# Performance work log

Hardware: AMD Instinct MI355X
Metric: run time of the kernel (lower is better)

Reference implementation:

```python
import jax, jax.numpy as jnp
from jax import lax
import numpy as np

OUTS = [5, 1, 2, 2, 1, 1, 1, 1]  # heatmap, conf, dxy, wh, dist, offset, severity, surface
OFFS = np.concatenate([[0], np.cumsum(OUTS)])
BN_EPS = 1e-5


def setup_inputs() -> dict:
    key = jax.random.key(0)
    ks = jax.random.split(key, 10)
    N, C, Hf, Wf = 16, 576, 12, 20
    f = jax.random.normal(ks[0], (N, C, Hf, Wf), jnp.float32)
    det_w1 = jax.random.normal(ks[1], (8, C, C, 3, 3), jnp.float32) * 0.02
    det_bn_g = 1.0 + 0.1 * jax.random.normal(ks[2], (8, C), jnp.float32)
    det_bn_b = 0.1 * jax.random.normal(ks[3], (8, C), jnp.float32)
    det_bn_m = 0.1 * jax.random.normal(ks[4], (8, C), jnp.float32)
    det_bn_v = jax.random.uniform(ks[5], (8, C), jnp.float32) + 0.5
    det_w2 = jax.random.normal(ks[6], (14, C), jnp.float32) * 0.05
    det_b2 = jax.random.normal(ks[7], (14,), jnp.float32) * 0.05
    lin_W = jax.random.normal(ks[8], (10, C), jnp.float32) * 0.05
    lin_b = jnp.zeros((10,), jnp.float32)
    return dict(f=f, det_w1=det_w1, det_bn_g=det_bn_g, det_bn_b=det_bn_b,
                det_bn_m=det_bn_m, det_bn_v=det_bn_v, det_w2=det_w2, det_b2=det_b2,
                lin_W=lin_W, lin_b=lin_b, frame_w=640, frame_h=384)


def _head(f, w1, g, b, m, v, w2, b2):
    # conv3x3 (no bias) -> BN (inference) -> SiLU -> conv1x1
    dn = ('NCHW', 'OIHW', 'NCHW')
    h = lax.conv_general_dilated(f, w1, (1, 1), 'SAME', dimension_numbers=dn)
    scale = g * lax.rsqrt(v + BN_EPS)
    h = h * scale[None, :, None, None] + (b - m * scale)[None, :, None, None]
    h = h * jax.nn.sigmoid(h)  # SiLU
    return jnp.einsum('nchw,oc->nohw', h, w2) + b2[None, :, None, None]


def _forward(f, det_w1, det_bn_g, det_bn_b, det_bn_m, det_bn_v, det_w2, det_b2,
             lin_W, lin_b, frame_w, frame_h, max_dets=20):
    N, C, Hf, Wf = f.shape
    eps = 1e-5
    # ---- legacy single-hazard head from pooled features ----
    f1 = f.mean(axis=(2, 3))                      # [N, 576]  (AdaptiveAvgPool2d(1))
    lin = f1 @ lin_W.T + lin_b                    # [N, 10]
    conf = jnp.clip(jax.nn.sigmoid(lin[:, 0:1]), eps, 1.0 - eps)
    type_log = lin[:, 1:6]
    dist_m = jax.nn.sigmoid(lin[:, 6:7]) * 3.0
    offset = jnp.tanh(lin[:, 7:8])
    severity = jnp.clip(jax.nn.sigmoid(lin[:, 8:9]), eps, 1.0 - eps)
    surface = jnp.clip(jax.nn.sigmoid(lin[:, 9:10]), eps, 1.0 - eps)
    type_id = jnp.argmax(type_log, axis=1, keepdims=True).astype(f.dtype)
    single_out = jnp.concatenate([conf, type_id, dist_m, offset, severity, surface], axis=1)

    # ---- dense per-pixel heads ----
    maps = []
    for i in range(8):
        o0, o1 = int(OFFS[i]), int(OFFS[i + 1])
        maps.append(_head(f, det_w1[i], det_bn_g[i], det_bn_b[i],
                          det_bn_m[i], det_bn_v[i], det_w2[o0:o1], det_b2[o0:o1]))
    heat = jax.nn.sigmoid(maps[0])                # [N,5,H,W]
    conf_d = jax.nn.sigmoid(maps[1])              # [N,1,H,W]
    dxy = jax.nn.sigmoid(maps[2])                 # [N,2,H,W]
    wh = jax.nn.sigmoid(maps[3])                  # [N,2,H,W]
    dist = jax.nn.sigmoid(maps[4]) * 3.0          # [N,1,H,W]
    offsm = jnp.tanh(maps[5])
    sev = jax.nn.sigmoid(maps[6])
    surf = jax.nn.sigmoid(maps[7])

    # ---- per-class topk decode ----
    score_flat = (conf_d * heat).reshape(N, 5, Hf * Wf)
    k = min(max_dets, Hf * Wf)
    topk_scores, topk_idx = lax.top_k(score_flat, k)          # [N,5,k]
    top_scores = topk_scores.reshape(N, -1)                    # [N,5k]
    top_class = jnp.broadcast_to(jnp.arange(5, dtype=f.dtype)[None, :, None], (N, 5, k)).reshape(N, -1)
    idx_flat = topk_idx.reshape(N, -1)                          # [N,5k]
    y_idx = (idx_flat // Wf).astype(f.dtype)
    x_idx = (idx_flat % Wf).astype(f.dtype)

    g1 = lambda m: jnp.take_along_axis(m.reshape(N, -1), idx_flat, axis=1)
    gx, gy = g1(dxy[:, 0]), g1(dxy[:, 1])
    gw, gh = g1(wh[:, 0]), g1(wh[:, 1])
    gdist, goffs = g1(dist), g1(offsm)
    gsev, gsurf = g1(sev), g1(surf)

    stride_x = frame_w / Wf
    stride_y = frame_h / Hf
    cx = jnp.clip(x_idx + gx, 0, Wf - 1) * stride_x
    cy = jnp.clip(y_idx + gy, 0, Hf - 1) * stride_y
    bw = jnp.clip(gw, 0, 1) * frame_w
    bh = jnp.clip(gh, 0, 1) * frame_h
    x1 = jnp.clip(cx - bw / 2, 0, frame_w - 1)
    y1 = jnp.clip(cy - bh / 2, 0, frame_h - 1)
    x2 = jnp.clip(cx + bw / 2, 0, frame_w - 1)
    y2 = jnp.clip(cy + bh / 2, 0, frame_h - 1)

    dets = jnp.stack([top_scores, top_class, gdist, goffs, gsev, gsurf, x1, y1, x2, y2], axis=-1)  # [N,5k,10]
    order = jnp.argsort(dets[:, :, 2], axis=-1)   # ascending distance (nearest first)
    dets_sorted = jnp.take_along_axis(dets, order[:, :, None], axis=1)
    dets_out = dets_sorted[:, :max_dets, :]        # [N,K,10]
    return single_out, dets_out


def reference(f, det_w1, det_bn_g, det_bn_b, det_bn_m, det_bn_v, det_w2, det_b2,
              lin_W, lin_b, frame_w, frame_h):
    return _forward(f, det_w1, det_bn_g, det_bn_b, det_bn_m, det_bn_v,
                    det_w2, det_b2, lin_W, lin_b, frame_w, frame_h)
```

## Files before the change

kernel.cpp:

```cpp
#include <hip/hip_runtime.h>
#include <math.h>

#define NB 16
#define CC 576
#define HH 12
#define WW 20
#define PP 240
#define MM 3840
#define NHEAD 8
#define HALO 22

typedef __attribute__((ext_vector_type(8))) short short8;
typedef __attribute__((ext_vector_type(4))) float floatx4;
typedef unsigned short ushort_t;

__device__ __forceinline__ float sigmoidf_(float x) {
    return 1.0f / (1.0f + expf(-x));
}
__device__ __forceinline__ unsigned short f2bf(float x) {
    union { float f; unsigned u; } v; v.f = x;
    unsigned r = v.u + 0x7fff + ((v.u >> 16) & 1);
    return (unsigned short)(r >> 16);
}
__device__ __forceinline__ float bf2f(unsigned short b) {
    union { float f; unsigned u; } v; v.u = ((unsigned)b) << 16;
    return v.f;
}

__device__ __forceinline__ void gl_lds16(const ushort_t* g, ushort_t* l) {
    __builtin_amdgcn_global_load_lds(
        (const __attribute__((address_space(1))) void*)g,
        (__attribute__((address_space(3))) void*)l, 16, 0, 0);
}

#define FENCED_BARRIER() do {                   \
    asm volatile("" ::: "memory");              \
    __builtin_amdgcn_sched_barrier(0);          \
    __builtin_amdgcn_s_barrier();               \
    __builtin_amdgcn_sched_barrier(0);          \
    asm volatile("" ::: "memory");              \
} while (0)

__global__ __launch_bounds__(256) void k_single(const float* __restrict__ f1sum,
                                                const float* __restrict__ linW,
                                                const float* __restrict__ linb,
                                                float* __restrict__ out) {
    int n = blockIdx.x;
    __shared__ float lin[10];
    int t = threadIdx.x;
    int lane = t & 63, wave = t >> 6;
    const float inv = 1.0f / PP;
    for (int o = wave; o < 10; o += 4) {
        const float* wrow = linW + o * CC;
        float s = 0.f;
        for (int c = lane; c < CC; c += 64)
            s = fmaf(f1sum[n * CC + c] * inv, wrow[c], s);
        #pragma unroll
        for (int off = 32; off; off >>= 1) s += __shfl_xor(s, off, 64);
        if (lane == 0) lin[o] = s + linb[o];
    }
    __syncthreads();
    if (t == 0) {
        const float eps = 1e-5f;
        float conf = sigmoidf_(lin[0]);
        conf = fminf(fmaxf(conf, eps), 1.f - eps);
        int best = 0; float bv = lin[1];
        #pragma unroll
        for (int j = 1; j < 5; ++j) { if (lin[1 + j] > bv) { bv = lin[1 + j]; best = j; } }
        float dist = 3.f * sigmoidf_(lin[6]);
        float offs = tanhf(lin[7]);
        float sev  = fminf(fmaxf(sigmoidf_(lin[8]), eps), 1.f - eps);
        float surf = fminf(fmaxf(sigmoidf_(lin[9]), eps), 1.f - eps);
        float* o = out + n * 6;
        o[0] = conf; o[1] = (float)best; o[2] = dist;
        o[3] = offs; o[4] = sev; o[5] = surf;
    }
}

__global__ __launch_bounds__(256) void k_prep_f(const float* __restrict__ f,
                                                ushort_t* __restrict__ fhi,
                                                ushort_t* __restrict__ flo,
                                                float* __restrict__ f1sum) {
    __shared__ float tile[32][33];
    int c0 = blockIdx.x * 32, p0 = blockIdx.y * 32, n = blockIdx.z;
    int tp = threadIdx.x & 31, tc8 = threadIdx.x >> 5;
    for (int cc = tc8; cc < 32; cc += 8) {
        int p = p0 + tp;
        tile[cc][tp] = (p < PP) ? f[((size_t)n * CC + c0 + cc) * PP + p] : 0.f;
    }
    __syncthreads();
    if (threadIdx.x < 32) {
        float s = 0.f;
        #pragma unroll
        for (int pp = 0; pp < 32; ++pp) s += tile[threadIdx.x][pp];
        atomicAdd(&f1sum[n * CC + c0 + threadIdx.x], s);
    }
    int tcw = threadIdx.x & 31, tpw = threadIdx.x >> 5;
    for (int pp = tpw; pp < 32; pp += 8) {
        int p = p0 + pp;
        if (p < PP) {
            float v = tile[tcw][pp];
            unsigned short hi = f2bf(v);
            size_t o = ((size_t)n * PP + p) * CC + c0 + tcw;
            fhi[o] = hi;
            flo[o] = f2bf(v - bf2f(hi));
        }
    }
}

__global__ __launch_bounds__(256) void k_prep_w(const float* __restrict__ w1,
                                                ushort_t* __restrict__ whi,
                                                ushort_t* __restrict__ wlo) {
    __shared__ float ws[CC * 9];
    int co = blockIdx.x % CC;
    int h  = blockIdx.x / CC;
    const float* src = w1 + ((size_t)(h * CC + co)) * CC * 9;
    for (int i = threadIdx.x; i < CC * 9 / 4; i += 256)
        *(float4*)(ws + i * 4) = *(const float4*)(src + i * 4);
    __syncthreads();
    for (int idx = threadIdx.x; idx < 9 * 72; idx += 256) {
        int tap = idx / 72, pos = idx - tap * 72;
        short8 vh, vl;
        #pragma unroll
        for (int e = 0; e < 8; ++e) {
            float v = ws[(pos * 8 + e) * 9 + tap];
            unsigned short hi = f2bf(v);
            vh[e] = (short)hi;
            vl[e] = (short)f2bf(v - bf2f(hi));
        }
        size_t ob = ((size_t)(h * 9 + tap) * CC + co) * CC + (size_t)pos * 8;
        *(short8*)(whi + ob) = vh;
        *(short8*)(wlo + ob) = vl;
    }
}

__global__ __launch_bounds__(256) void k_maps_init(float* __restrict__ maps,
                                                   const float* __restrict__ b2,
                                                   float* __restrict__ f1sum) {
    int i = blockIdx.x * 256 + threadIdx.x;
    if (i < NB * 14 * PP) {
        int o = (i / PP) % 14;
        maps[i] = b2[o];
    } else if (i < NB * 14 * PP + NB * CC) {
        f1sum[i - NB * 14 * PP] = 0.f;
    }
}

__global__ __launch_bounds__(256) void k_conv_mfma(
        const ushort_t* __restrict__ fhi, const ushort_t* __restrict__ flo,
        const ushort_t* __restrict__ whi, const ushort_t* __restrict__ wlo,
        const float* __restrict__ w2,
        const float* __restrict__ bng, const float* __restrict__ bnb,
        const float* __restrict__ bnm, const float* __restrict__ bnv,
        float* __restrict__ maps) {
    __shared__ __align__(16) ushort_t Ah[1216 * 8];
    __shared__ __align__(16) ushort_t Al[1216 * 8];
    __shared__ __align__(16) ushort_t Bh[2][256 * 8];
    __shared__ __align__(16) ushort_t Bl[2][256 * 8];
    __shared__ ushort_t rowmap[9 * 256];

    int t = threadIdx.x;

    int bid = blockIdx.x;
    int xcd = bid & 7;
    int q = bid >> 3;
    int mt = q % 15;
    int slice = (q / 15) * 8 + xcd;
    int m0 = mt * 256;
    int c0 = (slice % 9) * 64;
    int h  = slice / 9;

    int w = t >> 6, lane = t & 63;
    int quad = lane >> 4, l15 = lane & 15;
    int srow_lo = t & 15, sg = (t >> 4) & 3, srb = t >> 6;

    int bco = srb * 16 + srow_lo;
    size_t bconst = (size_t)(c0 + bco) * CC + sg * 8;
    const size_t hbase = (size_t)h * 9 * CC * CC;

    #pragma unroll
    for (int it = 0; it < 5; ++it) {
        int row = (srb + 4 * it) * 16 + srow_lo;
        if (row < 300) {
            ptrdiff_t mg = (ptrdiff_t)m0 - HALO + row;
            ptrdiff_t off = mg * CC + sg * 8;
            int cidx = 256 * it + t;
            gl_lds16(fhi + off, Ah + cidx * 8);
            gl_lds16(flo + off, Al + cidx * 8);
        }
    }
    gl_lds16(whi + hbase + bconst, &Bh[0][t * 8]);
    gl_lds16(wlo + hbase + bconst, &Bl[0][t * 8]);

    if (t < 32) {
        int arr = t >> 4, g = (t >> 2) & 3, rr = 12 + (t & 3);
        int idx = 18 * 64 + g * 16 + rr;
        short8 z = {0, 0, 0, 0, 0, 0, 0, 0};
        *(short8*)((arr ? Al : Ah) + idx * 8) = z;
    }
    for (int idx = t; idx < 9 * 256; idx += 256) {
        int tap = idx >> 8, ml = idx & 255;
        int m = m0 + ml;
        int p = m % PP;
        int y = p / WW, x = p - y * WW;
        int dy = tap / 3 - 1, dx = tap % 3 - 1;
        int yy = y + dy, xx = x + dx;
        int row;
        if ((unsigned)yy < (unsigned)HH && (unsigned)xx < (unsigned)WW)
            row = ml + dy * WW + dx + HALO;
        else
            row = 300 + (ml & 3);
        rowmap[idx] = (ushort_t)row;
    }
    __syncthreads();

    floatx4 acc[4][4];
    #pragma unroll
    for (int i = 0; i < 4; ++i)
        #pragma unroll
        for (int j = 0; j < 4; ++j) acc[i][j] = (floatx4){0.f, 0.f, 0.f, 0.f};

    for (int cib = 0; cib < 18; ++cib) {
        if (cib) {
            FENCED_BARRIER();
            #pragma unroll
            for (int it = 0; it < 5; ++it) {
                int row = (srb + 4 * it) * 16 + srow_lo;
                if (row < 300) {
                    ptrdiff_t mg = (ptrdiff_t)m0 - HALO + row;
                    ptrdiff_t off = mg * CC + cib * 32 + sg * 8;
                    int cidx = 256 * it + t;
                    gl_lds16(fhi + off, Ah + cidx * 8);
                    gl_lds16(flo + off, Al + cidx * 8);
                }
            }
        }
        for (int tap = 0; tap < 9; ++tap) {
            int bs = (cib + tap) & 1;
            __syncthreads();
            if (cib * 9 + tap + 1 < 162) {
                int ncib = (tap == 8) ? cib + 1 : cib;
                int ntap = (tap == 8) ? 0 : tap + 1;
                size_t src = hbase + (size_t)ntap * (CC * CC) + bconst
                           + (size_t)ncib * 32;
                gl_lds16(whi + src, &Bh[bs ^ 1][t * 8]);
                gl_lds16(wlo + src, &Bl[bs ^ 1][t * 8]);
            }

            short8 bh[4], bl[4], ah[4], al[4];
            #pragma unroll
            for (int j = 0; j < 4; ++j) {
                bh[j] = *(const short8*)(&Bh[bs][(j * 64 + lane) * 8]);
                bl[j] = *(const short8*)(&Bl[bs][(j * 64 + lane) * 8]);
            }
            #pragma unroll
            for (int i = 0; i < 4; ++i) {
                int r = rowmap[tap * 256 + w * 64 + i * 16 + l15];
                int a16 = ((r >> 4) * 64 + quad * 16 + (r & 15)) * 8;
                ah[i] = *(const short8*)(Ah + a16);
                al[i] = *(const short8*)(Al + a16);
            }
            #pragma unroll
            for (int i = 0; i < 4; ++i)
                #pragma unroll
                for (int j = 0; j < 4; ++j) {
                    acc[i][j] = __builtin_amdgcn_mfma_f32_16x16x32_bf16(
                        ah[i], bh[j], acc[i][j], 0, 0, 0);
                    acc[i][j] = __builtin_amdgcn_mfma_f32_16x16x32_bf16(
                        ah[i], bl[j], acc[i][j], 0, 0, 0);
                    acc[i][j] = __builtin_amdgcn_mfma_f32_16x16x32_bf16(
                        al[i], bh[j], acc[i][j], 0, 0, 0);
                }
        }
    }

    float scale[4], shift[4];
    #pragma unroll
    for (int j = 0; j < 4; ++j) {
        int c = h * CC + c0 + j * 16 + l15;
        float g_ = bng[c], bb = bnb[c], bm = bnm[c], bv = bnv[c];
        scale[j] = g_ / sqrtf(bv + 1e-5f);
        shift[j] = bb - bm * scale[j];
    }
    #pragma unroll
    for (int i = 0; i < 4; ++i)
        #pragma unroll
        for (int j = 0; j < 4; ++j)
            #pragma unroll
            for (int r = 0; r < 4; ++r) {
                float hx = fmaf(acc[i][j][r], scale[j], shift[j]);
                acc[i][j][r] = hx * sigmoidf_(hx);
            }

    static const int OFFo[NHEAD + 1] = {0, 5, 6, 8, 10, 11, 12, 13, 14};
    int o0 = OFFo[h], o1 = OFFo[h + 1];
    for (int o = o0; o < o1; ++o) {
        float w2v[4];
        #pragma unroll
        for (int j = 0; j < 4; ++j) w2v[j] = w2[o * CC + c0 + j * 16 + l15];
        float pv[4][4];
        #pragma unroll
        for (int i = 0; i < 4; ++i)
            #pragma unroll
            for (int r = 0; r < 4; ++r) {
                float s = 0.f;
                #pragma unroll
                for (int j = 0; j < 4; ++j) s = fmaf(acc[i][j][r], w2v[j], s);
                pv[i][r] = s;
            }
        #pragma unroll
        for (int off = 1; off < 16; off <<= 1)
            #pragma unroll
            for (int i = 0; i < 4; ++i)
                #pragma unroll
                for (int r = 0; r < 4; ++r)
                    pv[i][r] += __shfl_xor(pv[i][r], off, 64);
        if (l15 == 0) {
            #pragma unroll
            for (int i = 0; i < 4; ++i)
                #pragma unroll
                for (int r = 0; r < 4; ++r) {
                    int m = m0 + w * 64 + i * 16 + quad * 4 + r;
                    int n = m / PP, p = m - n * PP;
                    atomicAdd(&maps[(n * 14 + o) * PP + p], pv[i][r]);
                }
        }
    }
}

__global__ __launch_bounds__(256) void k_decode(
        const float* __restrict__ maps,
        const int* __restrict__ fw_p, const int* __restrict__ fh_p,
        float* __restrict__ out) {
    int n = blockIdx.x;
    int t = threadIdx.x;
    __shared__ float ms[14][PP];
    __shared__ float sconf[PP];
    __shared__ float cscore[100];
    __shared__ int   cidx[100];
    __shared__ float dets[100][10];
    __shared__ float dvals[100];

    const float* mp = maps + (size_t)n * 14 * PP;
    for (int idx = t; idx < 14 * PP; idx += 256) ms[idx / PP][idx % PP] = mp[idx];
    __syncthreads();
    if (t < PP) sconf[t] = sigmoidf_(ms[5][t]);
    __syncthreads();

    int wv = t >> 6, lane = t & 63;
    for (int cls = wv; cls < 5; cls += 4) {
        float v[4]; int pi[4];
        #pragma unroll
        for (int j = 0; j < 4; ++j) {
            int p = lane + 64 * j;
            pi[j] = p;
            v[j] = (p < PP) ? sconf[p] * sigmoidf_(ms[cls][p]) : -1e30f;
        }
        for (int r = 0; r < 20; ++r) {
            float bv = v[0]; int bi = pi[0];
            #pragma unroll
            for (int j = 1; j < 4; ++j)
                if (v[j] > bv || (v[j] == bv && pi[j] < bi)) { bv = v[j]; bi = pi[j]; }
            float rv = bv; int ri = bi;
            #pragma unroll
            for (int off = 32; off; off >>= 1) {
                float ov = __shfl_xor(rv, off, 64);
                int   oi = __shfl_xor(ri, off, 64);
                if (ov > rv || (ov == rv && oi < ri)) { rv = ov; ri = oi; }
            }
            if (lane == 0) { cscore[cls * 20 + r] = rv; cidx[cls * 20 + r] = ri; }
            #pragma unroll
            for (int j = 0; j < 4; ++j) if (pi[j] == ri) v[j] = -1e30f;
        }
    }
    __syncthreads();

    if (t < 100) {
        int cls = t / 20;
        int p = cidx[t];
        int yi = p / WW, xi = p - yi * WW;
        float gx = sigmoidf_(ms[6][p]),  gy = sigmoidf_(ms[7][p]);
        float gw = sigmoidf_(ms[8][p]),  gh = sigmoidf_(ms[9][p]);
        float gd = 3.f * sigmoidf_(ms[10][p]);
        float go = tanhf(ms[11][p]);
        float gs = sigmoidf_(ms[12][p]);
        float gf = sigmoidf_(ms[13][p]);
        float fw = (float)fw_p[0], fh = (float)fh_p[0];
        float sx = fw / (float)WW, sy = fh / (float)HH;
        float cx = fminf(fmaxf((float)xi + gx, 0.f), (float)WW - 1.f) * sx;
        float cy = fminf(fmaxf((float)yi + gy, 0.f), (float)HH - 1.f) * sy;
        float bw = fminf(fmaxf(gw, 0.f), 1.f) * fw;
        float bh = fminf(fmaxf(gh, 0.f), 1.f) * fh;
        float x1 = fminf(fmaxf(cx - bw * 0.5f, 0.f), fw - 1.f);
        float y1 = fminf(fmaxf(cy - bh * 0.5f, 0.f), fh - 1.f);
        float x2 = fminf(fmaxf(cx + bw * 0.5f, 0.f), fw - 1.f);
        float y2 = fminf(fmaxf(cy + bh * 0.5f, 0.f), fh - 1.f);
        dets[t][0] = cscore[t]; dets[t][1] = (float)cls;
        dets[t][2] = gd; dets[t][3] = go; dets[t][4] = gs; dets[t][5] = gf;
        dets[t][6] = x1; dets[t][7] = y1; dets[t][8] = x2; dets[t][9] = y2;
        dvals[t] = gd;
    }
    __syncthreads();
    if (t < 100) {
        float d = dvals[t];
        int rank = 0;
        for (int l = 0; l < 100; ++l) {
            float dl = dvals[l];
            rank += (dl < d) || (dl == d && l < t);
        }
        if (rank < 20) {
            float* o = out + 96 + ((size_t)n * 20 + rank) * 10;
            #pragma unroll
            for (int q = 0; q < 10; ++q) o[q] = dets[t][q];
        }
    }
}

extern "C" void kernel_launch(void* const* d_in, const int* in_sizes, int n_in,
                              void* d_out, int out_size, void* d_ws, size_t ws_size,
                              hipStream_t stream) {
    const float* f    = (const float*)d_in[0];
    const float* w1   = (const float*)d_in[1];
    const float* bng  = (const float*)d_in[2];
    const float* bnb  = (const float*)d_in[3];
    const float* bnm  = (const float*)d_in[4];
    const float* bnv  = (const float*)d_in[5];
    const float* w2   = (const float*)d_in[6];
    const float* b2   = (const float*)d_in[7];
    const float* linW = (const float*)d_in[8];
    const float* linb = (const float*)d_in[9];
    const int*   fw   = (const int*)d_in[10];
    const int*   fh   = (const int*)d_in[11];
    float* out = (float*)d_out;

    const size_t w_elems = (size_t)NHEAD * 9 * CC * CC;
    const size_t f_elems = (size_t)MM * CC;

    ushort_t* ws_whi = (ushort_t*)d_ws;
    ushort_t* ws_wlo = ws_whi + w_elems;
    ushort_t* ws_fhi = ws_wlo + w_elems;
    ushort_t* ws_flo = ws_fhi + f_elems;
    float*    ws_maps = (float*)(ws_flo + f_elems);
    float*    ws_f1sum = (float*)d_ws;

    k_maps_init<<<(NB * 14 * PP + NB * CC + 255) / 256, 256, 0, stream>>>(
        ws_maps, b2, ws_f1sum);
    k_prep_f<<<dim3(CC / 32, (PP + 31) / 32, NB), 256, 0, stream>>>(
        f, ws_fhi, ws_flo, ws_f1sum);
    k_single<<<NB, 256, 0, stream>>>(ws_f1sum, linW, linb, out);
    k_prep_w<<<NHEAD * CC, 256, 0, stream>>>(w1, ws_whi, ws_wlo);
    k_conv_mfma<<<dim3(15 * 9 * NHEAD), 256, 0, stream>>>(
        ws_fhi, ws_flo, ws_whi, ws_wlo, w2, bng, bnb, bnm, bnv, ws_maps);
    k_decode<<<NB, 256, 0, stream>>>(ws_maps, fw, fh, out);
}
```

Before: 793.8 us.

## Load conv weight fragments directly into registers with register double-buffering

The conv kernel no longer stages the B (weight) tiles through double-buffered LDS. Each lane now loads its own weight fragments straight from global memory into registers, prefetching the next tap's fragments while the current MFMAs run. This removes the per-tap __syncthreads, leaving barriers only when the activation tile is reloaded for each channel block. The MFMA sequence is also regrouped into three passes. Costs are more VGPRs for the prefetch buffers, and each wave now reads the shared weight tile from global/L2 separately, where before it was loaded once per block.

```diff
diff --git a/kernel.cpp b/kernel.cpp
--- a/kernel.cpp
+++ b/kernel.cpp
@@ -32,14 +32,6 @@
         (const __attribute__((address_space(1))) void*)g,
         (__attribute__((address_space(3))) void*)l, 16, 0, 0);
 }
-
-#define FENCED_BARRIER() do {                   \
-    asm volatile("" ::: "memory");              \
-    __builtin_amdgcn_sched_barrier(0);          \
-    __builtin_amdgcn_s_barrier();               \
-    __builtin_amdgcn_sched_barrier(0);          \
-    asm volatile("" ::: "memory");              \
-} while (0)
 
 __global__ __launch_bounds__(256) void k_single(const float* __restrict__ f1sum,
                                                 const float* __restrict__ linW,
@@ -155,8 +147,6 @@
         float* __restrict__ maps) {
     __shared__ __align__(16) ushort_t Ah[1216 * 8];
     __shared__ __align__(16) ushort_t Al[1216 * 8];
-    __shared__ __align__(16) ushort_t Bh[2][256 * 8];
-    __shared__ __align__(16) ushort_t Bl[2][256 * 8];
     __shared__ ushort_t rowmap[9 * 256];
 
     int t = threadIdx.x;
@@ -174,9 +164,9 @@
     int quad = lane >> 4, l15 = lane & 15;
     int srow_lo = t & 15, sg = (t >> 4) & 3, srb = t >> 6;
 
-    int bco = srb * 16 + srow_lo;
-    size_t bconst = (size_t)(c0 + bco) * CC + sg * 8;
     const size_t hbase = (size_t)h * 9 * CC * CC;
+    const ushort_t* wh_lane = whi + hbase + (size_t)(c0 + l15) * CC + quad * 8;
+    const ushort_t* wl_lane = wlo + hbase + (size_t)(c0 + l15) * CC + quad * 8;
 
     #pragma unroll
     for (int it = 0; it < 5; ++it) {
@@ -189,9 +179,6 @@
             gl_lds16(flo + off, Al + cidx * 8);
         }
     }
-    gl_lds16(whi + hbase + bconst, &Bh[0][t * 8]);
-    gl_lds16(wlo + hbase + bconst, &Bl[0][t * 8]);
-
     if (t < 32) {
         int arr = t >> 4, g = (t >> 2) & 3, rr = 12 + (t & 3);
         int idx = 18 * 64 + g * 16 + rr;
@@ -212,6 +199,14 @@
             row = 300 + (ml & 3);
         rowmap[idx] = (ushort_t)row;
     }
+
+    short8 cbh[4], cbl[4];
+    #pragma unroll
+    for (int j = 0; j < 4; ++j) {
+        cbh[j] = *(const short8*)(wh_lane + j * (16 * CC));
+        cbl[j] = *(const short8*)(wl_lane + j * (16 * CC));
+    }
+
     __syncthreads();
 
     floatx4 acc[4][4];
@@ -220,57 +215,76 @@
         #pragma unroll
         for (int j = 0; j < 4; ++j) acc[i][j] = (floatx4){0.f, 0.f, 0.f, 0.f};
 
-    for (int cib = 0; cib < 18; ++cib) {
-        if (cib) {
-            FENCED_BARRIER();
-            #pragma unroll
-            for (int it = 0; it < 5; ++it) {
-                int row = (srb + 4 * it) * 16 + srow_lo;
-                if (row < 300) {
-                    ptrdiff_t mg = (ptrdiff_t)m0 - HALO + row;
-                    ptrdiff_t off = mg * CC + cib * 32 + sg * 8;
-                    int cidx = 256 * it + t;
-                    gl_lds16(fhi + off, Ah + cidx * 8);
-                    gl_lds16(flo + off, Al + cidx * 8);
+    int cib = 0, tap = 0;
+    for (int step = 0; step < 162; ++step) {
+        short8 nbh[4], nbl[4];
+        int last = (step == 161);
+        if (!last) {
+            int ntap = (tap == 8) ? 0 : tap + 1;
+            int ncib = (tap == 8) ? cib + 1 : cib;
+            const ushort_t* bh_p = wh_lane + (size_t)ntap * (CC * CC) + ncib * 32;
+            const ushort_t* bl_p = wl_lane + (size_t)ntap * (CC * CC) + ncib * 32;
+            #pragma unroll
+            for (int j = 0; j < 4; ++j) {
+                nbh[j] = *(const short8*)(bh_p + j * (16 * CC));
+                nbl[j] = *(const short8*)(bl_p + j * (16 * CC));
+            }
+        }
+
+        short8 ah[4], al[4];
+        #pragma unroll
+        for (int i = 0; i < 4; ++i) {
+            int r = rowmap[tap * 256 + w * 64 + i * 16 + l15];
+            int a16 = ((r >> 4) * 64 + quad * 16 + (r & 15)) * 8;
+            ah[i] = *(const short8*)(Ah + a16);
+            al[i] = *(const short8*)(Al + a16);
+        }
+
+        #pragma unroll
+        for (int i = 0; i < 4; ++i)
+            #pragma unroll
+            for (int j = 0; j < 4; ++j)
+                acc[i][j] = __builtin_amdgcn_mfma_f32_16x16x32_bf16(
+                    ah[i], cbh[j], acc[i][j], 0, 0, 0);
+        #pragma unroll
+        for (int i = 0; i < 4; ++i)
+            #pragma unroll
+            for (int j = 0; j < 4; ++j)
+                acc[i][j] = __builtin_amdgcn_mfma_f32_16x16x32_bf16(
+                    ah[i], cbl[j], acc[i][j], 0, 0, 0);
+        #pragma unroll
+        for (int i = 0; i < 4; ++i)
+            #pragma unroll
+            for (int j = 0; j < 4; ++j)
+                acc[i][j] = __builtin_amdgcn_mfma_f32_16x16x32_bf16(
+                    al[i], cbh[j], acc[i][j], 0, 0, 0);
+
+        if (!last) {
+            #pragma unroll
+            for (int j = 0; j < 4; ++j) { cbh[j] = nbh[j]; cbl[j] = nbl[j]; }
+        }
+
+        if (tap == 8) {
+            tap = 0; ++cib;
+            if (cib < 18) {
+                asm volatile("" ::: "memory");
+                __builtin_amdgcn_s_barrier();
+                asm volatile("" ::: "memory");
+                #pragma unroll
+                for (int it = 0; it < 5; ++it) {
+                    int row = (srb + 4 * it) * 16 + srow_lo;
+                    if (row < 300) {
+                        ptrdiff_t mg = (ptrdiff_t)m0 - HALO + row;
+                        ptrdiff_t off = mg * CC + cib * 32 + sg * 8;
+                        int cidx = 256 * it + t;
+                        gl_lds16(fhi + off, Ah + cidx * 8);
+                        gl_lds16(flo + off, Al + cidx * 8);
+                    }
                 }
+                __syncthreads();
             }
-        }
-        for (int tap = 0; tap < 9; ++tap) {
-            int bs = (cib + tap) & 1;
-            __syncthreads();
-            if (cib * 9 + tap + 1 < 162) {
-                int ncib = (tap == 8) ? cib + 1 : cib;
-                int ntap = (tap == 8) ? 0 : tap + 1;
-                size_t src = hbase + (size_t)ntap * (CC * CC) + bconst
-                           + (size_t)ncib * 32;
-                gl_lds16(whi + src, &Bh[bs ^ 1][t * 8]);
-                gl_lds16(wlo + src, &Bl[bs ^ 1][t * 8]);
-            }
-
-            short8 bh[4], bl[4], ah[4], al[4];
-            #pragma unroll
-            for (int j = 0; j < 4; ++j) {
-                bh[j] = *(const short8*)(&Bh[bs][(j * 64 + lane) * 8]);
-                bl[j] = *(const short8*)(&Bl[bs][(j * 64 + lane) * 8]);
-            }
-            #pragma unroll
-            for (int i = 0; i < 4; ++i) {
-                int r = rowmap[tap * 256 + w * 64 + i * 16 + l15];
-                int a16 = ((r >> 4) * 64 + quad * 16 + (r & 15)) * 8;
-                ah[i] = *(const short8*)(Ah + a16);
-                al[i] = *(const short8*)(Al + a16);
-            }
-            #pragma unroll
-            for (int i = 0; i < 4; ++i)
-                #pragma unroll
-                for (int j = 0; j < 4; ++j) {
-                    acc[i][j] = __builtin_amdgcn_mfma_f32_16x16x32_bf16(
-                        ah[i], bh[j], acc[i][j], 0, 0, 0);
-                    acc[i][j] = __builtin_amdgcn_mfma_f32_16x16x32_bf16(
-                        ah[i], bl[j], acc[i][j], 0, 0, 0);
-                    acc[i][j] = __builtin_amdgcn_mfma_f32_16x16x32_bf16(
-                        al[i], bh[j], acc[i][j], 0, 0, 0);
-                }
+        } else {
+            ++tap;
         }
     }
 
```

Result: slower. 1.053 ms (+32.6%).
